# Optimization experiments

Measured on AMD Instinct MI355X. Metric: run time of the kernel, lower is better.

Reference implementation:

```python
import jax, jax.numpy as jnp
import numpy as np

N = 8192       # number of nodes (dense NxN attention)
F_IN = 256     # input feature dim
F_OUT = 64     # projected feature dim (F_prime)
NEG_SLOPE = 0.01  # nn.LeakyReLU default


def setup_inputs() -> dict:
    key = jax.random.key(0)
    k0, k1, k2, k3 = jax.random.split(key, 4)
    H = jax.random.normal(k0, (N, F_IN), dtype=jnp.float32)
    # dense 0/1 adjacency; force self-loops so every row has a nonzero denominator
    A = jax.random.randint(k1, (N, N), 0, 2, dtype=jnp.int32)
    A = jnp.maximum(A, jnp.eye(N, dtype=jnp.int32))
    # learned params: W : F_IN -> F_OUT (self.W), a : 2*F_OUT -> 1 (self.a)
    W = jax.random.normal(k2, (F_IN, F_OUT), dtype=jnp.float32) / np.sqrt(F_IN)
    bW = jnp.zeros((F_OUT,), dtype=jnp.float32)
    a_w = jax.random.normal(k3, (2 * F_OUT,), dtype=jnp.float32) / np.sqrt(2 * F_OUT)
    a_b = jnp.zeros((), dtype=jnp.float32)
    return {"H": H, "A": A, "W": W, "bW": bW, "a_w": a_w, "a_b": a_b}


def reference(H, A, W, bW, a_w, a_b):
    # Wh[i] = W(H[i])  -> [N, F_OUT]
    Wh = H @ W + bW
    # a([Wh_i ; Wh_j]) = a1.Wh_i + a2.Wh_j + a_b : decompose the concat-linear
    s_src = Wh @ a_w[:F_OUT]           # [N]
    s_tar = Wh @ a_w[F_OUT:]           # [N]
    logits = s_src[:, None] + s_tar[None, :] + a_b   # [N, N]
    # e_ij = exp(leaky_relu(logits))
    e = jnp.exp(jnp.where(logits >= 0, logits, NEG_SLOPE * logits))
    # denominator masks by adjacency (sum_j e_ij * A_ij), as in the original
    denom = jnp.sum(e * A.astype(e.dtype), axis=1, keepdims=True)  # [N, 1]
    alpha = e / denom                   # NOTE: numerator NOT masked (faithful)
    # H'_i = sigmoid(alpha_i @ Wh)
    return jax.nn.sigmoid(alpha @ Wh)   # [N, F_OUT]
```

## Files before the change

### kernel.cpp

```cpp
#include <hip/hip_runtime.h>
#include <hip/hip_bf16.h>

#define NN 8192
#define FIN 256
#define FOUT 64

__global__ __launch_bounds__(256) void k1_proj(
    const float* __restrict__ H, const float* __restrict__ W,
    const float* __restrict__ bW, const float* __restrict__ aw,
    const float* __restrict__ ab,
    float* __restrict__ Wh, float* __restrict__ s_src, float* __restrict__ t_tar,
    float* __restrict__ E1, float* __restrict__ E2, float* __restrict__ PP)
{
    __shared__ float Hs[16 * FIN];
    int tid = threadIdx.x;
    int i0 = blockIdx.x * 16;
    const float4* Hv = (const float4*)(H + (size_t)i0 * FIN);
    float4* Hsv = (float4*)Hs;
    for (int idx = tid; idx < 16 * FIN / 4; idx += 256) Hsv[idx] = Hv[idx];
    __syncthreads();
    int f = tid & 63, sub = tid >> 6;
    float a1f = aw[f], a2f = aw[64 + f];
    float b = bW[f];
    float acc0 = b, acc1 = b, acc2 = b, acc3 = b;
    for (int k = 0; k < FIN; ++k) {
        float w = W[k * FOUT + f];
        acc0 += Hs[(sub     ) * FIN + k] * w;
        acc1 += Hs[(sub +  4) * FIN + k] * w;
        acc2 += Hs[(sub +  8) * FIN + k] * w;
        acc3 += Hs[(sub + 12) * FIN + k] * w;
    }
    float accs[4] = {acc0, acc1, acc2, acc3};
    #pragma unroll
    for (int q = 0; q < 4; ++q) {
        int i = i0 + sub + 4 * q;
        float a = accs[q];
        Wh[(size_t)i * FOUT + f] = a;
        float v1 = a * a1f, v2 = a * a2f;
        #pragma unroll
        for (int o = 32; o > 0; o >>= 1) {
            v1 += __shfl_xor(v1, o);
            v2 += __shfl_xor(v2, o);
        }
        if (f == 0) {
            float s = v1 + ab[0];
            float t = v2;
            s_src[i] = s; t_tar[i] = t;
            E1[i] = __expf(s); E2[i] = __expf(0.01f * s);
            PP[2 * i]     = __expf(t);
            PP[2 * i + 1] = __expf(0.01f * t);
        }
    }
}

__global__ __launch_bounds__(256) void k2_rank(
    const float* __restrict__ t_tar, const float* __restrict__ s_src,
    int* __restrict__ sorted_idx, int* __restrict__ kidx)
{
    __shared__ float Ts[NN];
    int tid = threadIdx.x;
    const float4* tv = (const float4*)t_tar;
    float4* Tsv = (float4*)Ts;
    for (int idx = tid; idx < NN / 4; idx += 256) Tsv[idx] = tv[idx];
    __syncthreads();
    int wv = tid >> 6, lane = tid & 63;
    int g = blockIdx.x * 4 + wv;
    float tj = Ts[g];
    float thr = -s_src[g];
    int rank = 0, kc = 0;
    #pragma unroll 4
    for (int k = lane; k < NN; k += 64) {
        float tk = Ts[k];
        rank += (tk < tj || (tk == tj && k < g)) ? 1 : 0;
        kc   += (tk < thr) ? 1 : 0;
    }
    #pragma unroll
    for (int o = 32; o > 0; o >>= 1) {
        rank += __shfl_xor(rank, o);
        kc   += __shfl_xor(kc, o);
    }
    if (lane == 0) { sorted_idx[rank] = g; kidx[g] = kc; }
}

__global__ __launch_bounds__(64) void k3a_tots(
    const float* __restrict__ Wh, const float* __restrict__ PP,
    const int* __restrict__ sorted_idx,
    float* __restrict__ tots1, float* __restrict__ tots2)
{
    int c = blockIdx.x, f = threadIdx.x;
    float t1 = 0.f, t2 = 0.f;
    int m0 = c * 32;
    #pragma unroll 8
    for (int m = m0; m < m0 + 32; ++m) {
        int sj = sorted_idx[m];
        float wh = Wh[(size_t)sj * 64 + f];
        t1 += PP[2 * sj]     * wh;
        t2 += PP[2 * sj + 1] * wh;
    }
    tots1[c * 64 + f] = t1; tots2[c * 64 + f] = t2;
}

__global__ __launch_bounds__(1024) void k3b_scan(
    const float* __restrict__ tots1, const float* __restrict__ tots2,
    float* __restrict__ off1, float* __restrict__ off2,
    float* __restrict__ pre2, float* __restrict__ suf1)
{
    __shared__ float w1[16 * 64], w2[16 * 64];
    int tid = threadIdx.x, f = tid & 63, wv = tid >> 6;
    int c0 = wv * 16;
    float s1 = 0.f, s2 = 0.f;
    for (int c = c0; c < c0 + 16; ++c) { s1 += tots1[c * 64 + f]; s2 += tots2[c * 64 + f]; }
    w1[wv * 64 + f] = s1; w2[wv * 64 + f] = s2;
    __syncthreads();
    float o2 = 0.f;
    #pragma unroll
    for (int w = 0; w < 16; ++w) if (w < wv) o2 += w2[w * 64 + f];
    float run2 = o2;
    for (int c = c0; c < c0 + 16; ++c) { off2[c * 64 + f] = run2; run2 += tots2[c * 64 + f]; }
    if (wv == 15) pre2[(size_t)NN * 64 + f] = run2;
    float o1 = 0.f;
    #pragma unroll
    for (int w = 0; w < 16; ++w) if (w > wv) o1 += w1[w * 64 + f];
    float run1 = o1;
    for (int c = c0 + 15; c >= c0; --c) { off1[c * 64 + f] = run1; run1 += tots1[c * 64 + f]; }
    if (tid < 64) suf1[(size_t)NN * 64 + tid] = 0.f;
}

__global__ __launch_bounds__(64) void k3c_emit(
    const float* __restrict__ Wh, const float* __restrict__ PP,
    const int* __restrict__ sorted_idx,
    const float* __restrict__ off1, const float* __restrict__ off2,
    float* __restrict__ pre2, float* __restrict__ suf1)
{
    int c = blockIdx.x, f = threadIdx.x;
    int m0 = c * 32;
    float whr[32], p1r[32], p2r[32];
    #pragma unroll
    for (int q = 0; q < 32; ++q) {
        int sj = sorted_idx[m0 + q];
        whr[q] = Wh[(size_t)sj * 64 + f];
        p1r[q] = PP[2 * sj]; p2r[q] = PP[2 * sj + 1];
    }
    float run2 = off2[c * 64 + f];
    #pragma unroll
    for (int q = 0; q < 32; ++q) {
        pre2[(size_t)(m0 + q) * 64 + f] = run2;
        run2 += p2r[q] * whr[q];
    }
    float run1 = off1[c * 64 + f];
    #pragma unroll
    for (int q = 31; q >= 0; --q) {
        run1 += p1r[q] * whr[q];
        suf1[(size_t)(m0 + q) * 64 + f] = run1;
    }
}

__global__ __launch_bounds__(256) void k4_denom(
    const int* __restrict__ A, const float* __restrict__ PP,
    const float* __restrict__ E1, const float* __restrict__ E2,
    float* __restrict__ denom)
{
    int tid = threadIdx.x;
    int i0 = blockIdx.x * 8;
    float e1r[8], accA[8], accB[8];
    #pragma unroll
    for (int r = 0; r < 8; ++r) { e1r[r] = E1[i0 + r]; accA[r] = 0.f; accB[r] = 0.f; }
    const float4* PPv = (const float4*)PP;
    for (int jv = tid; jv < NN / 4; jv += 256) {
        float4 ppA = PPv[2 * jv];
        float4 ppB = PPv[2 * jv + 1];
        #pragma unroll
        for (int r = 0; r < 8; ++r) {
            const int4 a4 = *(const int4*)(A + (size_t)(i0 + r) * NN + jv * 4);
            float e1 = e1r[r];
            {
                bool c = e1 * ppA.x >= 1.0f;
                float af = (float)a4.x;
                accA[r] += af * (c ? ppA.x : 0.0f);
                accB[r] += af * (c ? 0.0f : ppA.y);
            }
            {
                bool c = e1 * ppA.z >= 1.0f;
                float af = (float)a4.y;
                accA[r] += af * (c ? ppA.z : 0.0f);
                accB[r] += af * (c ? 0.0f : ppA.w);
            }
            {
                bool c = e1 * ppB.x >= 1.0f;
                float af = (float)a4.z;
                accA[r] += af * (c ? ppB.x : 0.0f);
                accB[r] += af * (c ? 0.0f : ppB.y);
            }
            {
                bool c = e1 * ppB.z >= 1.0f;
                float af = (float)a4.w;
                accA[r] += af * (c ? ppB.z : 0.0f);
                accB[r] += af * (c ? 0.0f : ppB.w);
            }
        }
    }
    #pragma unroll
    for (int r = 0; r < 8; ++r) {
        #pragma unroll
        for (int o = 32; o > 0; o >>= 1) {
            accA[r] += __shfl_xor(accA[r], o);
            accB[r] += __shfl_xor(accB[r], o);
        }
    }
    __shared__ float red[4][8][2];
    int wv = tid >> 6;
    if ((tid & 63) == 0) {
        #pragma unroll
        for (int r = 0; r < 8; ++r) { red[wv][r][0] = accA[r]; red[wv][r][1] = accB[r]; }
    }
    __syncthreads();
    if (tid < 8) {
        float sA = red[0][tid][0] + red[1][tid][0] + red[2][tid][0] + red[3][tid][0];
        float sB = red[0][tid][1] + red[1][tid][1] + red[2][tid][1] + red[3][tid][1];
        denom[i0 + tid] = E1[i0 + tid] * sA + E2[i0 + tid] * sB;
    }
}

__global__ __launch_bounds__(256) void k5_out(
    const float* __restrict__ suf1, const float* __restrict__ pre2,
    const int* __restrict__ kidx, const float* __restrict__ E1,
    const float* __restrict__ E2, const float* __restrict__ denom,
    float* __restrict__ out)
{
    int tid = threadIdx.x;
    int f = tid & 63, sub = tid >> 6;
    int i = blockIdx.x * 4 + sub;
    int k = kidx[i];
    float num = E1[i] * suf1[(size_t)k * 64 + f] + E2[i] * pre2[(size_t)k * 64 + f];
    float x = num / denom[i];
    out[(size_t)i * 64 + f] = 1.0f / (1.0f + __expf(-x));
}

extern "C" void kernel_launch(void* const* d_in, const int* in_sizes, int n_in,
                              void* d_out, int out_size, void* d_ws, size_t ws_size,
                              hipStream_t stream) {
    const float* H  = (const float*)d_in[0];
    const int*   A  = (const int*)d_in[1];
    const float* W  = (const float*)d_in[2];
    const float* bW = (const float*)d_in[3];
    const float* aw = (const float*)d_in[4];
    const float* ab = (const float*)d_in[5];
    float* out = (float*)d_out;

    float* ws    = (float*)d_ws;
    float* Wh    = ws;
    float* s_src = Wh + 524288;
    float* t_tar = s_src + 8192;
    float* E1    = t_tar + 8192;
    float* E2    = E1 + 8192;
    float* PP    = E2 + 8192;
    float* denom = PP + 16384;
    float* pre2  = denom + 8192;
    float* suf1  = pre2 + 524352;
    float* tots1 = suf1 + 524352;
    float* tots2 = tots1 + 16384;
    float* off1  = tots2 + 16384;
    float* off2  = off1 + 16384;
    int* sorted_idx = (int*)(off2 + 16384);
    int* kidx       = sorted_idx + 8192;

    hipLaunchKernelGGL(k1_proj, dim3(512), dim3(256), 0, stream,
                       H, W, bW, aw, ab, Wh, s_src, t_tar, E1, E2, PP);
    hipLaunchKernelGGL(k2_rank, dim3(2048), dim3(256), 0, stream,
                       t_tar, s_src, sorted_idx, kidx);
    hipLaunchKernelGGL(k3a_tots, dim3(256), dim3(64), 0, stream,
                       Wh, PP, sorted_idx, tots1, tots2);
    hipLaunchKernelGGL(k3b_scan, dim3(1), dim3(1024), 0, stream,
                       tots1, tots2, off1, off2, pre2, suf1);
    hipLaunchKernelGGL(k3c_emit, dim3(256), dim3(64), 0, stream,
                       Wh, PP, sorted_idx, off1, off2, pre2, suf1);
    hipLaunchKernelGGL(k4_denom, dim3(1024), dim3(256), 0, stream,
                       A, PP, E1, E2, denom);
    hipLaunchKernelGGL(k5_out, dim3(2048), dim3(256), 0, stream,
                       suf1, pre2, kidx, E1, E2, denom, out);
}
```

Measured before the change: 418.2 us.

## Fuse rank and denominator kernels, drop per-element prefix emit, recompute in output

Merges the rank/threshold kernel and the adjacency-denominator kernel into one launch with block-index dispatch, so the compute-bound ranking work can overlap with the memory-bound A streaming. The rank path now handles 8 nodes per wavefront to amortize shared-memory reads. The full per-element prefix/suffix arrays (two N×64 buffers) are no longer materialized; the output kernel rebuilds the partial chunk sum from sorted indices and chunk offsets. A loads use nontemporal hints. This removes a kernel launch and roughly 4 MB of writes, but adds up to 32 gathered loads per output element.

```diff
diff --git a/kernel.cpp b/kernel.cpp
--- a/kernel.cpp
+++ b/kernel.cpp
@@ -4,6 +4,8 @@
 #define NN 8192
 #define FIN 256
 #define FOUT 64
+
+typedef int iv4 __attribute__((ext_vector_type(4)));
 
 __global__ __launch_bounds__(256) void k1_proj(
     const float* __restrict__ H, const float* __restrict__ W,
@@ -53,41 +55,126 @@
     }
 }
 
-__global__ __launch_bounds__(256) void k2_rank(
+__global__ __launch_bounds__(256) void k24(
+    const int* __restrict__ A, const float* __restrict__ PP,
+    const float* __restrict__ E1, const float* __restrict__ E2,
     const float* __restrict__ t_tar, const float* __restrict__ s_src,
-    int* __restrict__ sorted_idx, int* __restrict__ kidx)
-{
-    __shared__ float Ts[NN];
+    float* __restrict__ denom, int* __restrict__ sorted_idx, int* __restrict__ kidx)
+{
+    __shared__ float sh[NN];
     int tid = threadIdx.x;
-    const float4* tv = (const float4*)t_tar;
-    float4* Tsv = (float4*)Ts;
-    for (int idx = tid; idx < NN / 4; idx += 256) Tsv[idx] = tv[idx];
-    __syncthreads();
-    int wv = tid >> 6, lane = tid & 63;
-    int g = blockIdx.x * 4 + wv;
-    float tj = Ts[g];
-    float thr = -s_src[g];
-    int rank = 0, kc = 0;
-    #pragma unroll 4
-    for (int k = lane; k < NN; k += 64) {
-        float tk = Ts[k];
-        rank += (tk < tj || (tk == tj && k < g)) ? 1 : 0;
-        kc   += (tk < thr) ? 1 : 0;
-    }
-    #pragma unroll
-    for (int o = 32; o > 0; o >>= 1) {
-        rank += __shfl_xor(rank, o);
-        kc   += __shfl_xor(kc, o);
-    }
-    if (lane == 0) { sorted_idx[rank] = g; kidx[g] = kc; }
-}
-
-__global__ __launch_bounds__(64) void k3a_tots(
+    int b = blockIdx.x;
+    if (b < 1024) {
+        int i0 = b * 8;
+        float e1r[8], accA[8], accB[8];
+        #pragma unroll
+        for (int r = 0; r < 8; ++r) { e1r[r] = E1[i0 + r]; accA[r] = 0.f; accB[r] = 0.f; }
+        const float4* PPv = (const float4*)PP;
+        for (int jv = tid; jv < NN / 4; jv += 256) {
+            float4 ppA = PPv[2 * jv];
+            float4 ppB = PPv[2 * jv + 1];
+            #pragma unroll
+            for (int r = 0; r < 8; ++r) {
+                const iv4* ap = (const iv4*)(A + (size_t)(i0 + r) * NN + jv * 4);
+                iv4 a4 = __builtin_nontemporal_load(ap);
+                float e1 = e1r[r];
+                {
+                    bool c = e1 * ppA.x >= 1.0f;
+                    float af = (float)a4.x;
+                    accA[r] += af * (c ? ppA.x : 0.0f);
+                    accB[r] += af * (c ? 0.0f : ppA.y);
+                }
+                {
+                    bool c = e1 * ppA.z >= 1.0f;
+                    float af = (float)a4.y;
+                    accA[r] += af * (c ? ppA.z : 0.0f);
+                    accB[r] += af * (c ? 0.0f : ppA.w);
+                }
+                {
+                    bool c = e1 * ppB.x >= 1.0f;
+                    float af = (float)a4.z;
+                    accA[r] += af * (c ? ppB.x : 0.0f);
+                    accB[r] += af * (c ? 0.0f : ppB.y);
+                }
+                {
+                    bool c = e1 * ppB.z >= 1.0f;
+                    float af = (float)a4.w;
+                    accA[r] += af * (c ? ppB.z : 0.0f);
+                    accB[r] += af * (c ? 0.0f : ppB.w);
+                }
+            }
+        }
+        #pragma unroll
+        for (int r = 0; r < 8; ++r) {
+            #pragma unroll
+            for (int o = 32; o > 0; o >>= 1) {
+                accA[r] += __shfl_xor(accA[r], o);
+                accB[r] += __shfl_xor(accB[r], o);
+            }
+        }
+        int wv = tid >> 6;
+        if ((tid & 63) == 0) {
+            #pragma unroll
+            for (int r = 0; r < 8; ++r) {
+                sh[(wv * 8 + r) * 2]     = accA[r];
+                sh[(wv * 8 + r) * 2 + 1] = accB[r];
+            }
+        }
+        __syncthreads();
+        if (tid < 8) {
+            float sA = sh[tid * 2]      + sh[(8 + tid) * 2]      + sh[(16 + tid) * 2]      + sh[(24 + tid) * 2];
+            float sB = sh[tid * 2 + 1]  + sh[(8 + tid) * 2 + 1]  + sh[(16 + tid) * 2 + 1]  + sh[(24 + tid) * 2 + 1];
+            denom[i0 + tid] = E1[i0 + tid] * sA + E2[i0 + tid] * sB;
+        }
+    } else {
+        int rb = b - 1024;
+        const float4* tv = (const float4*)t_tar;
+        float4* shv = (float4*)sh;
+        for (int idx = tid; idx < NN / 4; idx += 256) shv[idx] = tv[idx];
+        __syncthreads();
+        int lane = tid & 63, wv = tid >> 6;
+        int g0 = rb * 32 + wv * 8;
+        float tj[8], thr[8];
+        int rank[8], kc[8];
+        #pragma unroll
+        for (int q = 0; q < 8; ++q) {
+            tj[q] = sh[g0 + q]; thr[q] = -s_src[g0 + q];
+            rank[q] = 0; kc[q] = 0;
+        }
+        for (int k = lane; k < NN; k += 64) {
+            float tk = sh[k];
+            #pragma unroll
+            for (int q = 0; q < 8; ++q) {
+                int g = g0 + q;
+                rank[q] += (tk < tj[q] || (tk == tj[q] && k < g)) ? 1 : 0;
+                kc[q]   += (tk < thr[q]) ? 1 : 0;
+            }
+        }
+        #pragma unroll
+        for (int q = 0; q < 8; ++q) {
+            #pragma unroll
+            for (int o = 32; o > 0; o >>= 1) {
+                rank[q] += __shfl_xor(rank[q], o);
+                kc[q]   += __shfl_xor(kc[q], o);
+            }
+        }
+        if (lane == 0) {
+            #pragma unroll
+            for (int q = 0; q < 8; ++q) {
+                sorted_idx[rank[q]] = g0 + q;
+                kidx[g0 + q] = kc[q];
+            }
+        }
+    }
+}
+
+__global__ __launch_bounds__(256) void k3a_tots(
     const float* __restrict__ Wh, const float* __restrict__ PP,
     const int* __restrict__ sorted_idx,
     float* __restrict__ tots1, float* __restrict__ tots2)
 {
-    int c = blockIdx.x, f = threadIdx.x;
+    int c = blockIdx.x * 4 + (threadIdx.x >> 6);
+    int f = threadIdx.x & 63;
     float t1 = 0.f, t2 = 0.f;
     int m0 = c * 32;
     #pragma unroll 8
@@ -102,8 +189,7 @@
 
 __global__ __launch_bounds__(1024) void k3b_scan(
     const float* __restrict__ tots1, const float* __restrict__ tots2,
-    float* __restrict__ off1, float* __restrict__ off2,
-    float* __restrict__ pre2, float* __restrict__ suf1)
+    float* __restrict__ off1, float* __restrict__ off2)
 {
     __shared__ float w1[16 * 64], w2[16 * 64];
     int tid = threadIdx.x, f = tid & 63, wv = tid >> 6;
@@ -117,121 +203,41 @@
     for (int w = 0; w < 16; ++w) if (w < wv) o2 += w2[w * 64 + f];
     float run2 = o2;
     for (int c = c0; c < c0 + 16; ++c) { off2[c * 64 + f] = run2; run2 += tots2[c * 64 + f]; }
-    if (wv == 15) pre2[(size_t)NN * 64 + f] = run2;
+    if (wv == 15) off2[256 * 64 + f] = run2;
     float o1 = 0.f;
     #pragma unroll
     for (int w = 0; w < 16; ++w) if (w > wv) o1 += w1[w * 64 + f];
     float run1 = o1;
     for (int c = c0 + 15; c >= c0; --c) { off1[c * 64 + f] = run1; run1 += tots1[c * 64 + f]; }
-    if (tid < 64) suf1[(size_t)NN * 64 + tid] = 0.f;
-}
-
-__global__ __launch_bounds__(64) void k3c_emit(
+    if (tid < 64) off1[256 * 64 + tid] = 0.f;
+}
+
+__global__ __launch_bounds__(256) void k5_out(
     const float* __restrict__ Wh, const float* __restrict__ PP,
     const int* __restrict__ sorted_idx,
     const float* __restrict__ off1, const float* __restrict__ off2,
-    float* __restrict__ pre2, float* __restrict__ suf1)
-{
-    int c = blockIdx.x, f = threadIdx.x;
-    int m0 = c * 32;
-    float whr[32], p1r[32], p2r[32];
-    #pragma unroll
-    for (int q = 0; q < 32; ++q) {
-        int sj = sorted_idx[m0 + q];
-        whr[q] = Wh[(size_t)sj * 64 + f];
-        p1r[q] = PP[2 * sj]; p2r[q] = PP[2 * sj + 1];
-    }
-    float run2 = off2[c * 64 + f];
-    #pragma unroll
-    for (int q = 0; q < 32; ++q) {
-        pre2[(size_t)(m0 + q) * 64 + f] = run2;
-        run2 += p2r[q] * whr[q];
-    }
-    float run1 = off1[c * 64 + f];
-    #pragma unroll
-    for (int q = 31; q >= 0; --q) {
-        run1 += p1r[q] * whr[q];
-        suf1[(size_t)(m0 + q) * 64 + f] = run1;
-    }
-}
-
-__global__ __launch_bounds__(256) void k4_denom(
-    const int* __restrict__ A, const float* __restrict__ PP,
-    const float* __restrict__ E1, const float* __restrict__ E2,
-    float* __restrict__ denom)
-{
-    int tid = threadIdx.x;
-    int i0 = blockIdx.x * 8;
-    float e1r[8], accA[8], accB[8];
-    #pragma unroll
-    for (int r = 0; r < 8; ++r) { e1r[r] = E1[i0 + r]; accA[r] = 0.f; accB[r] = 0.f; }
-    const float4* PPv = (const float4*)PP;
-    for (int jv = tid; jv < NN / 4; jv += 256) {
-        float4 ppA = PPv[2 * jv];
-        float4 ppB = PPv[2 * jv + 1];
-        #pragma unroll
-        for (int r = 0; r < 8; ++r) {
-            const int4 a4 = *(const int4*)(A + (size_t)(i0 + r) * NN + jv * 4);
-            float e1 = e1r[r];
-            {
-                bool c = e1 * ppA.x >= 1.0f;
-                float af = (float)a4.x;
-                accA[r] += af * (c ? ppA.x : 0.0f);
-                accB[r] += af * (c ? 0.0f : ppA.y);
-            }
-            {
-                bool c = e1 * ppA.z >= 1.0f;
-                float af = (float)a4.y;
-                accA[r] += af * (c ? ppA.z : 0.0f);
-                accB[r] += af * (c ? 0.0f : ppA.w);
-            }
-            {
-                bool c = e1 * ppB.x >= 1.0f;
-                float af = (float)a4.z;
-                accA[r] += af * (c ? ppB.x : 0.0f);
-                accB[r] += af * (c ? 0.0f : ppB.y);
-            }
-            {
-                bool c = e1 * ppB.z >= 1.0f;
-                float af = (float)a4.w;
-                accA[r] += af * (c ? ppB.z : 0.0f);
-                accB[r] += af * (c ? 0.0f : ppB.w);
-            }
-        }
-    }
-    #pragma unroll
-    for (int r = 0; r < 8; ++r) {
-        #pragma unroll
-        for (int o = 32; o > 0; o >>= 1) {
-            accA[r] += __shfl_xor(accA[r], o);
-            accB[r] += __shfl_xor(accB[r], o);
-        }
-    }
-    __shared__ float red[4][8][2];
-    int wv = tid >> 6;
-    if ((tid & 63) == 0) {
-        #pragma unroll
-        for (int r = 0; r < 8; ++r) { red[wv][r][0] = accA[r]; red[wv][r][1] = accB[r]; }
-    }
-    __syncthreads();
-    if (tid < 8) {
-        float sA = red[0][tid][0] + red[1][tid][0] + red[2][tid][0] + red[3][tid][0];
-        float sB = red[0][tid][1] + red[1][tid][1] + red[2][tid][1] + red[3][tid][1];
-        denom[i0 + tid] = E1[i0 + tid] * sA + E2[i0 + tid] * sB;
-    }
-}
-
-__global__ __launch_bounds__(256) void k5_out(
-    const float* __restrict__ suf1, const float* __restrict__ pre2,
     const int* __restrict__ kidx, const float* __restrict__ E1,
     const float* __restrict__ E2, const float* __restrict__ denom,
     float* __restrict__ out)
 {
     int tid = threadIdx.x;
-    int f = tid & 63, sub = tid >> 6;
-    int i = blockIdx.x * 4 + sub;
+    int f = tid & 63, wv = tid >> 6;
+    int i = blockIdx.x * 4 + wv;
     int k = kidx[i];
-    float num = E1[i] * suf1[(size_t)k * 64 + f] + E2[i] * pre2[(size_t)k * 64 + f];
+    int c = k >> 5, r = k & 31;
+    float pre = off2[c * 64 + f];
+    float suf = off1[c * 64 + f];
+    if (c < 256) {
+        int m0 = c * 32;
+        #pragma unroll 8
+        for (int q = 0; q < 32; ++q) {
+            int sj = sorted_idx[m0 + q];
+            float wh = Wh[(size_t)sj * 64 + f];
+            if (q < r) pre += PP[2 * sj + 1] * wh;
+            else       suf += PP[2 * sj] * wh;
+        }
+    }
+    float num = E1[i] * suf + E2[i] * pre;
     float x = num / denom[i];
     out[(size_t)i * 64 + f] = 1.0f / (1.0f + __expf(-x));
 }
@@ -255,27 +261,21 @@
     float* E2    = E1 + 8192;
     float* PP    = E2 + 8192;
     float* denom = PP + 16384;
-    float* pre2  = denom + 8192;
-    float* suf1  = pre2 + 524352;
-    float* tots1 = suf1 + 524352;
+    float* tots1 = denom + 8192;
     float* tots2 = tots1 + 16384;
     float* off1  = tots2 + 16384;
-    float* off2  = off1 + 16384;
-    int* sorted_idx = (int*)(off2 + 16384);
+    float* off2  = off1 + 16448;
+    int* sorted_idx = (int*)(off2 + 16448);
     int* kidx       = sorted_idx + 8192;
 
     hipLaunchKernelGGL(k1_proj, dim3(512), dim3(256), 0, stream,
                        H, W, bW, aw, ab, Wh, s_src, t_tar, E1, E2, PP);
-    hipLaunchKernelGGL(k2_rank, dim3(2048), dim3(256), 0, stream,
-                       t_tar, s_src, sorted_idx, kidx);
-    hipLaunchKernelGGL(k3a_tots, dim3(256), dim3(64), 0, stream,
+    hipLaunchKernelGGL(k24, dim3(1280), dim3(256), 0, stream,
+                       A, PP, E1, E2, t_tar, s_src, denom, sorted_idx, kidx);
+    hipLaunchKernelGGL(k3a_tots, dim3(64), dim3(256), 0, stream,
                        Wh, PP, sorted_idx, tots1, tots2);
     hipLaunchKernelGGL(k3b_scan, dim3(1), dim3(1024), 0, stream,
-                       tots1, tots2, off1, off2, pre2, suf1);
-    hipLaunchKernelGGL(k3c_emit, dim3(256), dim3(64), 0, stream,
-                       Wh, PP, sorted_idx, off1, off2, pre2, suf1);
-    hipLaunchKernelGGL(k4_denom, dim3(1024), dim3(256), 0, stream,
-                       A, PP, E1, E2, denom);
+                       tots1, tots2, off1, off2);
     hipLaunchKernelGGL(k5_out, dim3(2048), dim3(256), 0, stream,
-                       suf1, pre2, kidx, E1, E2, denom, out);
-}
+                       Wh, PP, sorted_idx, off1, off2, kidx, E1, E2, denom, out);
+}
```

Measured after the change: 438.6 us. 4.9% more time.
